# Kernel tuning notes

Measured on AMD Instinct MI355X. Metric: run time of the kernel, lower is better.

The kernel has to match this reference:

```python
import jax, jax.numpy as jnp
import numpy as np

LN_EPS = 1e-5

def _mha(xq, xkv, in_w, in_b, out_w, out_b, n_heads):
    # torch nn.MultiheadAttention, batch_first=True, dropout=0
    B, S, d = xq.shape
    T = xkv.shape[1]
    dh = d // n_heads
    wq, wk, wv = jnp.split(in_w, 3, axis=0)   # each [d, d]
    bq, bk, bv = jnp.split(in_b, 3)
    q = (xq @ wq.T + bq).reshape(B, S, n_heads, dh).transpose(0, 2, 1, 3)
    k = (xkv @ wk.T + bk).reshape(B, T, n_heads, dh).transpose(0, 2, 1, 3)
    v = (xkv @ wv.T + bv).reshape(B, T, n_heads, dh).transpose(0, 2, 1, 3)
    scores = jnp.einsum('bhsd,bhtd->bhst', q, k) / jnp.sqrt(jnp.asarray(dh, xq.dtype))
    attn = jax.nn.softmax(scores, axis=-1)    # explicit [B,H,S,T] weights (need_weights=True path)
    o = jnp.einsum('bhst,bhtd->bhsd', attn, v)
    o = o.transpose(0, 2, 1, 3).reshape(B, S, d)
    return o @ out_w.T + out_b

def _ln(x, g, b):
    mu = jnp.mean(x, axis=-1, keepdims=True)
    var = jnp.mean(jnp.square(x - mu), axis=-1, keepdims=True)
    return (x - mu) / jnp.sqrt(var + LN_EPS) * g + b

def setup_inputs() -> dict:
    key = jax.random.key(0)
    B, S, T, d, ff = 4, 1024, 1024, 1024, 4096
    ks = jax.random.split(key, 10)
    s = 0.02
    return {
        'x': jax.random.normal(ks[0], (B, S, d), jnp.float32),
        'mem': jax.random.normal(ks[1], (B, T, d), jnp.float32),
        'sa_in_w': jax.random.normal(ks[2], (3 * d, d), jnp.float32) * s,
        'sa_in_b': jnp.zeros((3 * d,), jnp.float32),
        'sa_out_w': jax.random.normal(ks[3], (d, d), jnp.float32) * s,
        'sa_out_b': jnp.zeros((d,), jnp.float32),
        'ca_in_w': jax.random.normal(ks[4], (3 * d, d), jnp.float32) * s,
        'ca_in_b': jnp.zeros((3 * d,), jnp.float32),
        'ca_out_w': jax.random.normal(ks[5], (d, d), jnp.float32) * s,
        'ca_out_b': jnp.zeros((d,), jnp.float32),
        'ff_w1': jax.random.normal(ks[6], (ff, d), jnp.float32) * s,
        'ff_b1': jnp.zeros((ff,), jnp.float32),
        'ff_w2': jax.random.normal(ks[7], (d, ff), jnp.float32) * s,
        'ff_b2': jnp.zeros((d,), jnp.float32),
        'ln1_g': jnp.ones((d,), jnp.float32), 'ln1_b': jnp.zeros((d,), jnp.float32),
        'ln2_g': jnp.ones((d,), jnp.float32), 'ln2_b': jnp.zeros((d,), jnp.float32),
        'ln3_g': jnp.ones((d,), jnp.float32), 'ln3_b': jnp.zeros((d,), jnp.float32),
        'n_heads': 16,
    }

def reference(x, mem, sa_in_w, sa_in_b, sa_out_w, sa_out_b,
              ca_in_w, ca_in_b, ca_out_w, ca_out_b,
              ff_w1, ff_b1, ff_w2, ff_b2,
              ln1_g, ln1_b, ln2_g, ln2_b, ln3_g, ln3_b, n_heads):
    sa = _mha(x, x, sa_in_w, sa_in_b, sa_out_w, sa_out_b, n_heads)
    x = _ln(x + sa, ln1_g, ln1_b)
    ca = _mha(x, mem, ca_in_w, ca_in_b, ca_out_w, ca_out_b, n_heads)
    x = _ln(x + ca, ln2_g, ln2_b)
    h = jax.nn.gelu(x @ ff_w1.T + ff_b1, approximate=False)  # torch nn.GELU default = exact erf
    ff = h @ ff_w2.T + ff_b2
    return _ln(x + ff, ln3_g, ln3_b)
```

## Files before the change

### kernel.cpp

```cpp
#include <hip/hip_runtime.h>
#include <cstddef>

#define D_MODEL 1024
#define SEQ     1024
#define BATCH   4
#define NHEAD   16
#define DH      64
#define FFDIM   4096
#define NTOK    (BATCH*SEQ)

typedef float f32x4  __attribute__((ext_vector_type(4)));
typedef short bf16x8 __attribute__((ext_vector_type(8)));

static __device__ __forceinline__ unsigned short f2bf(float x){
  union { float f; unsigned u; } v; v.f = x;
  unsigned r = v.u + 0x7fffu + ((v.u >> 16) & 1u);
  return (unsigned short)(r >> 16);
}

static __device__ __forceinline__ float bf2f(unsigned short h){
  union { unsigned u; float f; } v; v.u = ((unsigned)h) << 16; return v.f;
}

static __device__ __forceinline__ void gl_lds16(const void* g, void* l){
  __builtin_amdgcn_global_load_lds((const __attribute__((address_space(1))) void*)g,
                                   (__attribute__((address_space(3))) void*)l, 16, 0, 0);
}

static __device__ __forceinline__ int2 swz_tile(int gx, int RX, int RY){
  int id = blockIdx.y * gx + blockIdx.x;
  int x = id & 7, s = id >> 3;
  int nrx = gx / RX;
  int bx = (x % nrx) * RX + (s % RX);
  int by = (x / nrx) * RY + (s / RX);
  return make_int2(bx, by);
}

struct CvtJobs {
  const float* src[8];
  unsigned short* dst[8];
  int n[8];
};

__global__ __launch_bounds__(256) void cvt_kernel(CvtJobs jobs){
  int seg = blockIdx.y;
  const float* s = jobs.src[seg];
  unsigned short* d = jobs.dst[seg];
  int n = jobs.n[seg];
  int stride = gridDim.x * 256 * 4;
  for (int i = (blockIdx.x*256 + threadIdx.x)*4; i < n; i += stride){
    float4 v = *(const float4*)(s + i);
    ushort4 o;
    o.x = f2bf(v.x); o.y = f2bf(v.y); o.z = f2bf(v.z); o.w = f2bf(v.w);
    *(ushort4*)(d + i) = o;
  }
}

static __device__ __forceinline__ int cidx(int row, int col){
  return row*128 + (((col >> 3) ^ (row & 15)) << 3) + (col & 7);
}

template<int EPI>
static __device__ __forceinline__ void gemm_core(
    unsigned short* smem,
    const unsigned short* __restrict__ A,
    const unsigned short* __restrict__ B,
    const float* __restrict__ bias,
    void* __restrict__ out0,
    unsigned short* __restrict__ vt,
    int N, int K, int kbeg, int kend, int row0, int col0,
    int split, int ldout)
{
  unsigned short* As = smem;
  unsigned short* Bs = smem + 128*64;
  const int tid  = threadIdx.x;
  const int w    = tid >> 6, lane = tid & 63;
  const int quad = lane >> 4, l15 = lane & 15;
  const int lr   = lane >> 3, lc = lane & 7;
  const int csrc = lc ^ lr;
  const int sw   = l15 & 7;
  const int wm = (w >> 1) * 64, wn = (w & 1) * 64;

  f32x4 acc[4][4];
  const f32x4 zero4 = {0.f, 0.f, 0.f, 0.f};
  #pragma unroll
  for (int i=0;i<4;i++)
    #pragma unroll
    for (int j=0;j<4;j++)
      acc[i][j] = zero4;

  const unsigned short* Ag = A + (size_t)(row0 + lr)*K + csrc*8;
  const unsigned short* Bg = B + (size_t)(col0 + lr)*K + csrc*8;

  for (int k0 = kbeg; k0 < kend; k0 += 64){
    #pragma unroll
    for (int i=0;i<4;i++){
      gl_lds16(Ag + (size_t)(i*32 + w*8)*K + k0, &As[i*2048 + w*512]);
      gl_lds16(Bg + (size_t)(i*32 + w*8)*K + k0, &Bs[i*2048 + w*512]);
    }
    __syncthreads();
    #pragma unroll
    for (int ks=0; ks<2; ks++){
      bf16x8 af[4], bfr[4];
      #pragma unroll
      for (int i=0;i<4;i++)
        af[i] = *(const bf16x8*)&As[(wm + i*16 + l15)*64 + ((ks*4 + quad) ^ sw)*8];
      #pragma unroll
      for (int j=0;j<4;j++)
        bfr[j] = *(const bf16x8*)&Bs[(wn + j*16 + l15)*64 + ((ks*4 + quad) ^ sw)*8];
      #pragma unroll
      for (int i=0;i<4;i++)
        #pragma unroll
        for (int j=0;j<4;j++)
          acc[i][j] = __builtin_amdgcn_mfma_f32_16x16x32_bf16(af[i], bfr[j], acc[i][j], 0, 0, 0);
    }
    __syncthreads();
  }

  float bj[4];
  #pragma unroll
  for (int j=0;j<4;j++) bj[j] = bias[col0 + wn + j*16 + l15];

  const bool vtile = (EPI == 5) && (col0 >= split);
  unsigned short* Cs = smem;

  #pragma unroll
  for (int i=0;i<4;i++){
    #pragma unroll
    for (int r=0;r<4;r++){
      int lrow = wm + i*16 + quad*4 + r;
      #pragma unroll
      for (int j=0;j<4;j++){
        int lcol = wn + j*16 + l15;
        float v = acc[i][j][r] + bj[j];
        if (EPI == 2){
          float t = 0.7978845608f * (v + 0.044715f * v * v * v);
          float e = __expf(2.f * t);
          float th = 1.f - 2.f * __builtin_amdgcn_rcpf(e + 1.f);
          v = 0.5f * v * (1.f + th);
        }
        if (vtile) Cs[cidx(lcol, lrow)] = f2bf(v);
        else       Cs[cidx(lrow, lcol)] = f2bf(v);
      }
    }
  }
  __syncthreads();

  const int ld = (EPI == 5) ? ldout : N;
  #pragma unroll
  for (int p=0;p<2;p++){
    int c = p*64 + (tid >> 2);
    unsigned short* dst;
    if (!vtile){
      dst = (unsigned short*)out0 + (size_t)(row0 + c)*ld + col0;
    } else {
      int colg = (col0 - split) + c;
      int hh = colg >> 6, dd = colg & 63;
      int bb = row0 >> 10, t0 = row0 & 1023;
      dst = vt + ((size_t)(bb*NHEAD + hh)*DH + dd)*SEQ + t0;
    }
    #pragma unroll
    for (int k=0;k<4;k++){
      int m = (tid & 3) + k*4;
      bf16x8 val = *(const bf16x8*)&Cs[c*128 + ((m ^ (c & 15)) << 3)];
      *(bf16x8*)(dst + m*8) = val;
    }
  }
}

template<int EPI>
__global__ __launch_bounds__(256) void gemm_swz(
    const unsigned short* A, const unsigned short* B, const float* bias,
    void* out0, int N, int K, int RX, int RY)
{
  __shared__ __align__(16) unsigned short smem[2*128*64];
  int2 t = swz_tile(gridDim.x, RX, RY);
  gemm_core<EPI>(smem, A, B, bias, out0, nullptr, N, K, 0, K,
                 t.y*128, t.x*128, 0, 0);
}

__global__ __launch_bounds__(256) void gemm_kv(
    const unsigned short* xb, const unsigned short* memb,
    const unsigned short* wsa, const unsigned short* wca,
    const float* bsa, const float* bca,
    unsigned short* ksa, unsigned short* vtsa,
    unsigned short* kca, unsigned short* vtca)
{
  __shared__ __align__(16) unsigned short smem[2*128*64];
  const int id = blockIdx.x;
  const bool sa = id < 512;
  const int hid = id & 511;
  const int x = hid & 7, s = hid >> 3;
  const int bx = (x & 1)*8 + (s & 7);
  const int by = (x >> 1)*8 + (s >> 3);
  gemm_core<5>(smem, sa ? xb : memb, sa ? wsa : wca, sa ? bsa : bca,
               sa ? ksa : kca, sa ? vtsa : vtca,
               2048, 1024, 0, 1024, by*128, bx*128, 1024, 1024);
}

__global__ __launch_bounds__(256) void gemm_split(
    const unsigned short* A, const unsigned short* B, const float* bias,
    unsigned short* outA, unsigned short* outB, int N, int K)
{
  __shared__ __align__(16) unsigned short smem[2*128*64];
  int2 t = swz_tile(gridDim.x, 4, 8);
  int kseg = K >> 1;
  int kbeg = blockIdx.z * kseg;
  unsigned short* o = blockIdx.z ? outB : outA;
  gemm_core<1>(smem, A, B, bias, o, nullptr, N, K, kbeg, kbeg + kseg,
               t.y*128, t.x*128, 0, 0);
}

__global__ __launch_bounds__(256) void gemm_split4(
    const unsigned short* A, const unsigned short* B, const float* bias,
    unsigned short* o0, unsigned short* o1, unsigned short* o2, unsigned short* o3,
    int N, int K)
{
  __shared__ __align__(16) unsigned short smem[2*128*64];
  int2 t = swz_tile(gridDim.x, 4, 8);
  int kseg = K >> 2;
  int kbeg = blockIdx.z * kseg;
  unsigned short* o = (blockIdx.z == 0) ? o0 : (blockIdx.z == 1) ? o1
                    : (blockIdx.z == 2) ? o2 : o3;
  gemm_core<1>(smem, A, B, bias, o, nullptr, N, K, kbeg, kbeg + kseg,
               t.y*128, t.x*128, 0, 0);
}

__global__ __launch_bounds__(256) void attn_kernel(
    const unsigned short* __restrict__ Xa,
    const unsigned short* __restrict__ Wq,
    const float* __restrict__ bq,
    const unsigned short* __restrict__ Kp,
    const unsigned short* __restrict__ Vt,
    unsigned short* __restrict__ O)
{
  __shared__ __align__(16) unsigned short Qs[128*64];
  __shared__ __align__(16) unsigned short Ks[64*64];
  __shared__ __align__(16) unsigned short Vs[64*64];
  __shared__ __align__(16) unsigned short Ps[4*32*72];

  const int tid  = threadIdx.x;
  const int w    = tid >> 6, lane = tid & 63;
  const int quad = lane >> 4, l15 = lane & 15;
  const int lr   = lane >> 3, lc = lane & 7;
  const int csrc = lc ^ lr;
  const int sw   = l15 & 7;
  const int id = blockIdx.x;
  const int xc = id & 7, s = id >> 3;
  const int bh = xc*8 + (s >> 3), qt = s & 7;
  const int b = bh >> 4, h = bh & 15;
  const int q0   = qt * 128;
  const int tok0 = b * SEQ;
  const int hoff = h * DH;

  f32x4 qacc[2][4];
  const f32x4 zero4 = {0.f, 0.f, 0.f, 0.f};
  #pragma unroll
  for (int qi=0;qi<2;qi++)
    #pragma unroll
    for (int dj=0;dj<4;dj++)
      qacc[qi][dj] = zero4;

  const unsigned short* Ag = Xa + (size_t)(tok0 + q0 + lr)*1024 + csrc*8;
  const unsigned short* Wg = Wq + (size_t)(hoff + lr)*1024 + csrc*8;

  for (int k0 = 0; k0 < 1024; k0 += 64){
    #pragma unroll
    for (int i=0;i<4;i++)
      gl_lds16(Ag + (size_t)(i*32 + w*8)*1024 + k0, &Qs[i*2048 + w*512]);
    #pragma unroll
    for (int i=0;i<2;i++)
      gl_lds16(Wg + (size_t)(i*32 + w*8)*1024 + k0, &Ks[i*2048 + w*512]);
    __syncthreads();
    #pragma unroll
    for (int ks=0; ks<2; ks++){
      bf16x8 af[2], bfr[4];
      #pragma unroll
      for (int qi=0;qi<2;qi++)
        af[qi] = *(const bf16x8*)&Qs[(w*32 + qi*16 + l15)*64 + ((ks*4 + quad) ^ sw)*8];
      #pragma unroll
      for (int dj=0;dj<4;dj++)
        bfr[dj] = *(const bf16x8*)&Ks[(dj*16 + l15)*64 + ((ks*4 + quad) ^ sw)*8];
      #pragma unroll
      for (int qi=0;qi<2;qi++)
        #pragma unroll
        for (int dj=0;dj<4;dj++)
          qacc[qi][dj] = __builtin_amdgcn_mfma_f32_16x16x32_bf16(af[qi], bfr[dj], qacc[qi][dj], 0, 0, 0);
    }
    __syncthreads();
  }

  {
    float biasv[4];
    #pragma unroll
    for (int dj=0;dj<4;dj++) biasv[dj] = bq[hoff + dj*16 + l15];
    #pragma unroll
    for (int qi=0;qi<2;qi++)
      #pragma unroll
      for (int dj=0;dj<4;dj++)
        #pragma unroll
        for (int r=0;r<4;r++){
          int q = w*32 + qi*16 + quad*4 + r;
          int d = dj*16 + l15;
          Qs[q*64 + (((d>>3) ^ (q&7))<<3) + (d&7)] = f2bf(qacc[qi][dj][r] + biasv[dj]);
        }
  }
  __syncthreads();

  bf16x8 qb[2][2];
  #pragma unroll
  for (int qi=0;qi<2;qi++){
    int row = w*32 + qi*16 + l15;
    qb[qi][0] = *(const bf16x8*)&Qs[row*64 + ((0 + quad) ^ sw)*8];
    qb[qi][1] = *(const bf16x8*)&Qs[row*64 + ((4 + quad) ^ sw)*8];
  }

  float lsum[2] = {0.f, 0.f};
  f32x4 oacc[2][4];
  #pragma unroll
  for (int qi=0;qi<2;qi++)
    #pragma unroll
    for (int dt=0;dt<4;dt++)
      oacc[qi][dt] = zero4;

  unsigned short* pw = &Ps[w*32*72];

  for (int kc = 0; kc < SEQ/64; ++kc){
    __syncthreads();
    #pragma unroll
    for (int i=0;i<2;i++){
      int r = i*32 + w*8 + lr;
      gl_lds16(Kp + (size_t)(tok0 + kc*64 + r)*1024 + hoff + csrc*8, &Ks[i*2048 + w*512]);
      gl_lds16(Vt + ((size_t)bh*DH + r)*SEQ + kc*64 + csrc*8,        &Vs[i*2048 + w*512]);
    }
    __syncthreads();

    #pragma unroll
    for (int tj=0;tj<4;tj++){
      bf16x8 ka0 = *(const bf16x8*)&Ks[(tj*16 + l15)*64 + ((0 + quad) ^ sw)*8];
      bf16x8 ka1 = *(const bf16x8*)&Ks[(tj*16 + l15)*64 + ((4 + quad) ^ sw)*8];
      #pragma unroll
      for (int qi=0;qi<2;qi++){
        f32x4 z = zero4;
        __builtin_amdgcn_s_setprio(1);
        z = __builtin_amdgcn_mfma_f32_16x16x32_bf16(ka0, qb[qi][0], z, 0, 0, 0);
        z = __builtin_amdgcn_mfma_f32_16x16x32_bf16(ka1, qb[qi][1], z, 0, 0, 0);
        __builtin_amdgcn_s_setprio(0);
        float p0 = __expf(z[0] * 0.125f);
        float p1 = __expf(z[1] * 0.125f);
        float p2 = __expf(z[2] * 0.125f);
        float p3 = __expf(z[3] * 0.125f);
        lsum[qi] += (p0 + p1) + (p2 + p3);
        short4 pk;
        pk.x = (short)f2bf(p0); pk.y = (short)f2bf(p1);
        pk.z = (short)f2bf(p2); pk.w = (short)f2bf(p3);
        *(short4*)&pw[(qi*16 + l15)*72 + tj*16 + quad*4] = pk;
      }
    }

    __builtin_amdgcn_s_setprio(1);
    #pragma unroll
    for (int qi=0;qi<2;qi++){
      bf16x8 pa0 = *(const bf16x8*)&pw[(qi*16 + l15)*72 + quad*8];
      bf16x8 pa1 = *(const bf16x8*)&pw[(qi*16 + l15)*72 + 32 + quad*8];
      #pragma unroll
      for (int dt=0;dt<4;dt++){
        bf16x8 vb0 = *(const bf16x8*)&Vs[(dt*16 + l15)*64 + ((0 + quad) ^ sw)*8];
        bf16x8 vb1 = *(const bf16x8*)&Vs[(dt*16 + l15)*64 + ((4 + quad) ^ sw)*8];
        oacc[qi][dt] = __builtin_amdgcn_mfma_f32_16x16x32_bf16(pa0, vb0, oacc[qi][dt], 0, 0, 0);
        oacc[qi][dt] = __builtin_amdgcn_mfma_f32_16x16x32_bf16(pa1, vb1, oacc[qi][dt], 0, 0, 0);
      }
    }
    __builtin_amdgcn_s_setprio(0);
  }

  #pragma unroll
  for (int qi=0;qi<2;qi++){
    lsum[qi] += __shfl_xor(lsum[qi], 16);
    lsum[qi] += __shfl_xor(lsum[qi], 32);
  }

  __syncthreads();
  unsigned short* OB = Ps;
  #pragma unroll
  for (int qi=0;qi<2;qi++){
    #pragma unroll
    for (int r=0;r<4;r++){
      float lv = __shfl(lsum[qi], quad*4 + r);
      float rinv = __builtin_amdgcn_rcpf(lv);
      int q = w*32 + qi*16 + quad*4 + r;
      #pragma unroll
      for (int dt=0;dt<4;dt++){
        int d = dt*16 + l15;
        OB[q*64 + (((d>>3) ^ (q&7))<<3) + (d&7)] = f2bf(oacc[qi][dt][r] * rinv);
      }
    }
  }
  __syncthreads();
  {
    int q = tid >> 1;
    unsigned short* dst = O + (size_t)(tok0 + q0 + q)*D_MODEL + hoff;
    #pragma unroll
    for (int k=0;k<4;k++){
      int m = (tid & 1)*4 + k;
      bf16x8 val = *(const bf16x8*)&OB[q*64 + ((m ^ (q & 7)) << 3)];
      *(bf16x8*)(dst + m*8) = val;
    }
  }
}

__global__ __launch_bounds__(256) void ln_kernel(
    const float* __restrict__ resid,
    const unsigned short* __restrict__ d1,
    const unsigned short* __restrict__ d2,
    const unsigned short* __restrict__ d3,
    const unsigned short* __restrict__ d4,
    const float* __restrict__ g, const float* __restrict__ beta,
    float* __restrict__ outf, unsigned short* __restrict__ outb)
{
  const int row = blockIdx.x;
  const int t = threadIdx.x;
  const size_t base = (size_t)row * D_MODEL;
  float4 a = *(const float4*)(resid + base + t*4);
  ushort4 p4 = *(const ushort4*)(d1 + base + t*4);
  ushort4 q4 = *(const ushort4*)(d2 + base + t*4);
  float v0 = a.x + bf2f(p4.x) + bf2f(q4.x);
  float v1 = a.y + bf2f(p4.y) + bf2f(q4.y);
  float v2 = a.z + bf2f(p4.z) + bf2f(q4.z);
  float v3 = a.w + bf2f(p4.w) + bf2f(q4.w);
  if (d3){
    ushort4 r4 = *(const ushort4*)(d3 + base + t*4);
    ushort4 s4 = *(const ushort4*)(d4 + base + t*4);
    v0 += bf2f(r4.x) + bf2f(s4.x);
    v1 += bf2f(r4.y) + bf2f(s4.y);
    v2 += bf2f(r4.z) + bf2f(s4.z);
    v3 += bf2f(r4.w) + bf2f(s4.w);
  }
  float s1 = v0+v1+v2+v3;
  float s2 = v0*v0+v1*v1+v2*v2+v3*v3;
  #pragma unroll
  for (int off=32; off>0; off>>=1){
    s1 += __shfl_down(s1, off);
    s2 += __shfl_down(s2, off);
  }
  __shared__ float red[8];
  const int wid = t >> 6;
  if ((t & 63) == 0){ red[wid*2] = s1; red[wid*2+1] = s2; }
  __syncthreads();
  s1 = red[0]+red[2]+red[4]+red[6];
  s2 = red[1]+red[3]+red[5]+red[7];
  float mean = s1 * (1.f/1024.f);
  float var  = s2 * (1.f/1024.f) - mean*mean;
  float rstd = rsqrtf(var + 1e-5f);
  float4 gg = *(const float4*)(g + t*4);
  float4 bb = *(const float4*)(beta + t*4);
  float y0 = (v0-mean)*rstd*gg.x + bb.x;
  float y1 = (v1-mean)*rstd*gg.y + bb.y;
  float y2 = (v2-mean)*rstd*gg.z + bb.z;
  float y3 = (v3-mean)*rstd*gg.w + bb.w;
  if (outf) *(float4*)(outf + base + t*4) = make_float4(y0,y1,y2,y3);
  if (outb){
    ushort4 o;
    o.x = f2bf(y0); o.y = f2bf(y1); o.z = f2bf(y2); o.w = f2bf(y3);
    *(ushort4*)(outb + base + t*4) = o;
  }
}

extern "C" void kernel_launch(void* const* d_in, const int* in_sizes, int n_in,
                              void* d_out, int out_size, void* d_ws, size_t ws_size,
                              hipStream_t stream)
{
  const float* x        = (const float*)d_in[0];
  const float* mem      = (const float*)d_in[1];
  const float* sa_in_w  = (const float*)d_in[2];
  const float* sa_in_b  = (const float*)d_in[3];
  const float* sa_out_w = (const float*)d_in[4];
  const float* sa_out_b = (const float*)d_in[5];
  const float* ca_in_w  = (const float*)d_in[6];
  const float* ca_in_b  = (const float*)d_in[7];
  const float* ca_out_w = (const float*)d_in[8];
  const float* ca_out_b = (const float*)d_in[9];
  const float* ff_w1    = (const float*)d_in[10];
  const float* ff_b1    = (const float*)d_in[11];
  const float* ff_w2    = (const float*)d_in[12];
  const float* ff_b2    = (const float*)d_in[13];
  const float* ln1_g    = (const float*)d_in[14];
  const float* ln1_b    = (const float*)d_in[15];
  const float* ln2_g    = (const float*)d_in[16];
  const float* ln2_b    = (const float*)d_in[17];
  const float* ln3_g    = (const float*)d_in[18];
  const float* ln3_b    = (const float*)d_in[19];

  char* base = (char*)d_ws;
  size_t off = 0;
  auto alloc = [&](size_t bytes) -> void* {
    void* r = base + off;
    off += (bytes + 255) & ~(size_t)255;
    return r;
  };
  unsigned short* xb     = (unsigned short*)alloc((size_t)NTOK*1024*2);
  unsigned short* memb   = (unsigned short*)alloc((size_t)NTOK*1024*2);
  unsigned short* wsain  = (unsigned short*)alloc((size_t)3072*1024*2);
  unsigned short* wsaout = (unsigned short*)alloc((size_t)1024*1024*2);
  unsigned short* wcain  = (unsigned short*)alloc((size_t)3072*1024*2);
  unsigned short* wcaout = (unsigned short*)alloc((size_t)1024*1024*2);
  unsigned short* wff1   = (unsigned short*)alloc((size_t)4096*1024*2);
  unsigned short* wff2   = (unsigned short*)alloc((size_t)4096*1024*2);
  unsigned short* qkvbuf = (unsigned short*)alloc((size_t)NTOK*3072*2);
  unsigned short* attnb  = (unsigned short*)alloc((size_t)NTOK*1024*2);
  float*          proj   = (float*)alloc((size_t)NTOK*1024*4);
  float*          x1f    = (float*)alloc((size_t)NTOK*1024*4);
  unsigned short* x1b    = (unsigned short*)alloc((size_t)NTOK*1024*2);
  float*          x2f    = (float*)alloc((size_t)NTOK*1024*4);
  unsigned short* x2b    = (unsigned short*)alloc((size_t)NTOK*1024*2);

  unsigned short* ksa  = qkvbuf;
  unsigned short* vtsa = qkvbuf + (size_t)NTOK*1024;
  unsigned short* kca  = qkvbuf + (size_t)NTOK*2048;
  unsigned short* vtca = (unsigned short*)x2f;
  unsigned short* hbuf = qkvbuf;
  unsigned short* pA   = (unsigned short*)proj;
  unsigned short* pB   = (unsigned short*)xb;
  unsigned short* q0p  = (unsigned short*)proj;
  unsigned short* q1p  = (unsigned short*)proj + (size_t)NTOK*1024;
  unsigned short* q2p  = (unsigned short*)x1f;
  unsigned short* q3p  = (unsigned short*)x1f + (size_t)NTOK*1024;

  CvtJobs jobs;
  jobs.src[0]=x;        jobs.dst[0]=xb;     jobs.n[0]=NTOK*1024;
  jobs.src[1]=mem;      jobs.dst[1]=memb;   jobs.n[1]=NTOK*1024;
  jobs.src[2]=sa_in_w;  jobs.dst[2]=wsain;  jobs.n[2]=3072*1024;
  jobs.src[3]=sa_out_w; jobs.dst[3]=wsaout; jobs.n[3]=1024*1024;
  jobs.src[4]=ca_in_w;  jobs.dst[4]=wcain;  jobs.n[4]=3072*1024;
  jobs.src[5]=ca_out_w; jobs.dst[5]=wcaout; jobs.n[5]=1024*1024;
  jobs.src[6]=ff_w1;    jobs.dst[6]=wff1;   jobs.n[6]=4096*1024;
  jobs.src[7]=ff_w2;    jobs.dst[7]=wff2;   jobs.n[7]=4096*1024;
  cvt_kernel<<<dim3(1024,8), 256, 0, stream>>>(jobs);

  gemm_kv<<<1024, 256, 0, stream>>>(xb, memb,
                                    wsain + (size_t)1024*1024, wcain + (size_t)1024*1024,
                                    sa_in_b + 1024, ca_in_b + 1024,
                                    ksa, vtsa, kca, vtca);

  attn_kernel<<<512, 256, 0, stream>>>(xb, wsain, sa_in_b, ksa, vtsa, attnb);
  gemm_split<<<dim3(8,32,2), 256, 0, stream>>>(attnb, wsaout, sa_out_b, pA, pB, 1024, 1024);
  ln_kernel<<<NTOK, 256, 0, stream>>>(x, pA, pB, nullptr, nullptr, ln1_g, ln1_b, x1f, x1b);

  attn_kernel<<<512, 256, 0, stream>>>(x1b, wcain, ca_in_b, kca, vtca, attnb);
  gemm_split<<<dim3(8,32,2), 256, 0, stream>>>(attnb, wcaout, ca_out_b, pA, pB, 1024, 1024);
  ln_kernel<<<NTOK, 256, 0, stream>>>(x1f, pA, pB, nullptr, nullptr, ln2_g, ln2_b, x2f, x2b);

  gemm_swz<2><<<dim3(32,32), 256, 0, stream>>>(x2b, wff1, ff_b1, hbuf, 4096, 1024, 8, 16);
  gemm_split4<<<dim3(8,32,4), 256, 0, stream>>>(hbuf, wff2, ff_b2, q0p, q1p, q2p, q3p, 1024, 4096);
  ln_kernel<<<NTOK, 256, 0, stream>>>(x2f, q0p, q1p, q2p, q3p, ln3_g, ln3_b, (float*)d_out, nullptr);
}
```

Measured before the change: 461.6 us.

## Double-buffer Q-projection and K/V tile loads in fused attention kernel

```diff
diff --git a/kernel.cpp b/kernel.cpp
--- a/kernel.cpp
+++ b/kernel.cpp
@@ -26,6 +26,10 @@
   __builtin_amdgcn_global_load_lds((const __attribute__((address_space(1))) void*)g,
                                    (__attribute__((address_space(3))) void*)l, 16, 0, 0);
 }
+
+#define WAITV(n) asm volatile("s_waitcnt vmcnt(" #n ")" ::: "memory")
+#define SBAR()   __builtin_amdgcn_s_barrier()
+#define SCHED0() __builtin_amdgcn_sched_barrier(0)
 
 static __device__ __forceinline__ int2 swz_tile(int gx, int RX, int RY){
   int id = blockIdx.y * gx + blockIdx.x;
@@ -253,8 +257,9 @@
   const int tok0 = b * SEQ;
   const int hoff = h * DH;
 
+  const f32x4 zero4 = {0.f, 0.f, 0.f, 0.f};
+
   f32x4 qacc[2][4];
-  const f32x4 zero4 = {0.f, 0.f, 0.f, 0.f};
   #pragma unroll
   for (int qi=0;qi<2;qi++)
     #pragma unroll
@@ -264,30 +269,45 @@
   const unsigned short* Ag = Xa + (size_t)(tok0 + q0 + lr)*1024 + csrc*8;
   const unsigned short* Wg = Wq + (size_t)(hoff + lr)*1024 + csrc*8;
 
-  for (int k0 = 0; k0 < 1024; k0 += 64){
+  auto stageQ = [&](int k0, unsigned short* dA, unsigned short* dW){
     #pragma unroll
     for (int i=0;i<4;i++)
-      gl_lds16(Ag + (size_t)(i*32 + w*8)*1024 + k0, &Qs[i*2048 + w*512]);
+      gl_lds16(Ag + (size_t)(i*32 + w*8)*1024 + k0, &dA[i*2048 + w*512]);
     #pragma unroll
     for (int i=0;i<2;i++)
-      gl_lds16(Wg + (size_t)(i*32 + w*8)*1024 + k0, &Ks[i*2048 + w*512]);
-    __syncthreads();
+      gl_lds16(Wg + (size_t)(i*32 + w*8)*1024 + k0, &dW[i*2048 + w*512]);
+  };
+
+  auto computeQ = [&](const unsigned short* As_, const unsigned short* Ws_){
     #pragma unroll
     for (int ks=0; ks<2; ks++){
       bf16x8 af[2], bfr[4];
       #pragma unroll
       for (int qi=0;qi<2;qi++)
-        af[qi] = *(const bf16x8*)&Qs[(w*32 + qi*16 + l15)*64 + ((ks*4 + quad) ^ sw)*8];
+        af[qi] = *(const bf16x8*)&As_[(w*32 + qi*16 + l15)*64 + ((ks*4 + quad) ^ sw)*8];
       #pragma unroll
       for (int dj=0;dj<4;dj++)
-        bfr[dj] = *(const bf16x8*)&Ks[(dj*16 + l15)*64 + ((ks*4 + quad) ^ sw)*8];
+        bfr[dj] = *(const bf16x8*)&Ws_[(dj*16 + l15)*64 + ((ks*4 + quad) ^ sw)*8];
       #pragma unroll
       for (int qi=0;qi<2;qi++)
         #pragma unroll
         for (int dj=0;dj<4;dj++)
           qacc[qi][dj] = __builtin_amdgcn_mfma_f32_16x16x32_bf16(af[qi], bfr[dj], qacc[qi][dj], 0, 0, 0);
     }
-    __syncthreads();
+  };
+
+  stageQ(0, Qs, Ks);
+  for (int t=0; t<8; t++){
+    const int k0 = t*128;
+    stageQ(k0+64, Ps, Vs);
+    WAITV(6); SBAR(); SCHED0();
+    computeQ(Qs, Ks);
+    SCHED0(); SBAR();
+    if (t < 7){ stageQ(k0+128, Qs, Ks); WAITV(6); }
+    else      { WAITV(0); }
+    SBAR(); SCHED0();
+    computeQ(Ps, Vs);
+    SCHED0(); SBAR();
   }
 
   {
@@ -314,6 +334,7 @@
     qb[qi][0] = *(const bf16x8*)&Qs[row*64 + ((0 + quad) ^ sw)*8];
     qb[qi][1] = *(const bf16x8*)&Qs[row*64 + ((4 + quad) ^ sw)*8];
   }
+  __syncthreads();
 
   float lsum[2] = {0.f, 0.f};
   f32x4 oacc[2][4];
@@ -324,21 +345,23 @@
       oacc[qi][dt] = zero4;
 
   unsigned short* pw = &Ps[w*32*72];
-
-  for (int kc = 0; kc < SEQ/64; ++kc){
-    __syncthreads();
+  unsigned short* K1 = Qs;
+  unsigned short* V1 = Qs + 64*64;
+
+  auto stageKV = [&](int kc, unsigned short* kb, unsigned short* vb){
     #pragma unroll
     for (int i=0;i<2;i++){
       int r = i*32 + w*8 + lr;
-      gl_lds16(Kp + (size_t)(tok0 + kc*64 + r)*1024 + hoff + csrc*8, &Ks[i*2048 + w*512]);
-      gl_lds16(Vt + ((size_t)bh*DH + r)*SEQ + kc*64 + csrc*8,        &Vs[i*2048 + w*512]);
-    }
-    __syncthreads();
-
+      gl_lds16(Kp + (size_t)(tok0 + kc*64 + r)*1024 + hoff + csrc*8, &kb[i*2048 + w*512]);
+      gl_lds16(Vt + ((size_t)bh*DH + r)*SEQ + kc*64 + csrc*8,        &vb[i*2048 + w*512]);
+    }
+  };
+
+  auto computeKC = [&](const unsigned short* kb, const unsigned short* vb){
     #pragma unroll
     for (int tj=0;tj<4;tj++){
-      bf16x8 ka0 = *(const bf16x8*)&Ks[(tj*16 + l15)*64 + ((0 + quad) ^ sw)*8];
-      bf16x8 ka1 = *(const bf16x8*)&Ks[(tj*16 + l15)*64 + ((4 + quad) ^ sw)*8];
+      bf16x8 ka0 = *(const bf16x8*)&kb[(tj*16 + l15)*64 + ((0 + quad) ^ sw)*8];
+      bf16x8 ka1 = *(const bf16x8*)&kb[(tj*16 + l15)*64 + ((4 + quad) ^ sw)*8];
       #pragma unroll
       for (int qi=0;qi<2;qi++){
         f32x4 z = zero4;
@@ -357,7 +380,6 @@
         *(short4*)&pw[(qi*16 + l15)*72 + tj*16 + quad*4] = pk;
       }
     }
-
     __builtin_amdgcn_s_setprio(1);
     #pragma unroll
     for (int qi=0;qi<2;qi++){
@@ -365,13 +387,27 @@
       bf16x8 pa1 = *(const bf16x8*)&pw[(qi*16 + l15)*72 + 32 + quad*8];
       #pragma unroll
       for (int dt=0;dt<4;dt++){
-        bf16x8 vb0 = *(const bf16x8*)&Vs[(dt*16 + l15)*64 + ((0 + quad) ^ sw)*8];
-        bf16x8 vb1 = *(const bf16x8*)&Vs[(dt*16 + l15)*64 + ((4 + quad) ^ sw)*8];
+        bf16x8 vb0 = *(const bf16x8*)&vb[(dt*16 + l15)*64 + ((0 + quad) ^ sw)*8];
+        bf16x8 vb1 = *(const bf16x8*)&vb[(dt*16 + l15)*64 + ((4 + quad) ^ sw)*8];
         oacc[qi][dt] = __builtin_amdgcn_mfma_f32_16x16x32_bf16(pa0, vb0, oacc[qi][dt], 0, 0, 0);
         oacc[qi][dt] = __builtin_amdgcn_mfma_f32_16x16x32_bf16(pa1, vb1, oacc[qi][dt], 0, 0, 0);
       }
     }
     __builtin_amdgcn_s_setprio(0);
+  };
+
+  stageKV(0, Ks, Vs);
+  for (int t=0; t<8; t++){
+    const int kcA = 2*t;
+    stageKV(kcA+1, K1, V1);
+    WAITV(4); SBAR(); SCHED0();
+    computeKC(Ks, Vs);
+    SCHED0(); SBAR();
+    if (t < 7){ stageKV(kcA+2, Ks, Vs); WAITV(4); }
+    else      { WAITV(0); }
+    SBAR(); SCHED0();
+    computeKC(K1, V1);
+    SCHED0(); SBAR();
   }
 
   #pragma unroll
```

Result: no change. 466.6 us (+1.1%).

## Use 256x256 tile GEMM with 512 threads for KV, FFN1 and FFN2

Applied to the files above, without the earlier changes.

```diff
diff --git a/kernel.cpp b/kernel.cpp
--- a/kernel.cpp
+++ b/kernel.cpp
@@ -26,6 +26,11 @@
   __builtin_amdgcn_global_load_lds((const __attribute__((address_space(1))) void*)g,
                                    (__attribute__((address_space(3))) void*)l, 16, 0, 0);
 }
+
+#define WAITV(n) asm volatile("s_waitcnt vmcnt(" #n ")" ::: "memory")
+#define WAITL0() asm volatile("s_waitcnt lgkmcnt(0)" ::: "memory")
+#define SBAR()   __builtin_amdgcn_s_barrier()
+#define SCHED0() __builtin_amdgcn_sched_barrier(0)
 
 static __device__ __forceinline__ int2 swz_tile(int gx, int RX, int RY){
   int id = blockIdx.y * gx + blockIdx.x;
@@ -121,17 +126,152 @@
   #pragma unroll
   for (int j=0;j<4;j++) bj[j] = bias[col0 + wn + j*16 + l15];
 
+  unsigned short* Cs = smem;
+
+  #pragma unroll
+  for (int i=0;i<4;i++){
+    #pragma unroll
+    for (int r=0;r<4;r++){
+      int lrow = wm + i*16 + quad*4 + r;
+      #pragma unroll
+      for (int j=0;j<4;j++){
+        int lcol = wn + j*16 + l15;
+        float v = acc[i][j][r] + bj[j];
+        Cs[cidx(lrow, lcol)] = f2bf(v);
+      }
+    }
+  }
+  __syncthreads();
+
+  const int ld = N;
+  #pragma unroll
+  for (int p=0;p<2;p++){
+    int c = p*64 + (tid >> 2);
+    unsigned short* dst = (unsigned short*)out0 + (size_t)(row0 + c)*ld + col0;
+    #pragma unroll
+    for (int k=0;k<4;k++){
+      int m = (tid & 3) + k*4;
+      bf16x8 val = *(const bf16x8*)&Cs[c*128 + ((m ^ (c & 15)) << 3)];
+      *(bf16x8*)(dst + m*8) = val;
+    }
+  }
+}
+
+__global__ __launch_bounds__(256) void gemm_split(
+    const unsigned short* A, const unsigned short* B, const float* bias,
+    unsigned short* outA, unsigned short* outB, int N, int K)
+{
+  __shared__ __align__(16) unsigned short smem[2*128*64];
+  int2 t = swz_tile(gridDim.x, 4, 8);
+  int kseg = K >> 1;
+  int kbeg = blockIdx.z * kseg;
+  unsigned short* o = blockIdx.z ? outB : outA;
+  gemm_core<1>(smem, A, B, bias, o, nullptr, N, K, kbeg, kbeg + kseg,
+               t.y*128, t.x*128, 0, 0);
+}
+
+template<int EPI>
+static __device__ __forceinline__ void gemm256_core(
+    unsigned short* smem,
+    const unsigned short* __restrict__ A,
+    const unsigned short* __restrict__ B,
+    const float* __restrict__ bias,
+    void* __restrict__ out0,
+    unsigned short* __restrict__ vt,
+    int N, int K, int kbeg, int kend, int row0, int col0,
+    int split, int ldout)
+{
+  const int tid  = threadIdx.x;
+  const int w    = tid >> 6, lane = tid & 63;
+  const int quad = lane >> 4, l15 = lane & 15;
+  const int lr   = lane >> 3, lc = lane & 7;
+  const int csrc = lc ^ lr;
+  const int sw   = l15 & 7;
+  const int wr   = w >> 2, wc = w & 3;
+
+  f32x4 acc[8][4];
+  const f32x4 zero4 = {0.f, 0.f, 0.f, 0.f};
+  #pragma unroll
+  for (int i=0;i<8;i++)
+    #pragma unroll
+    for (int j=0;j<4;j++)
+      acc[i][j] = zero4;
+
+  const unsigned short* Ag = A + (size_t)(row0 + lr)*K + csrc*8;
+  const unsigned short* Bg = B + (size_t)(col0 + lr)*K + csrc*8;
+
+  auto stageT = [&](int k0, unsigned short* dst){
+    #pragma unroll
+    for (int i=0;i<4;i++)
+      gl_lds16(Ag + (size_t)(i*64 + w*8)*K + k0, dst + i*4096 + w*512);
+    #pragma unroll
+    for (int i=0;i<4;i++)
+      gl_lds16(Bg + (size_t)(i*64 + w*8)*K + k0, dst + 256*64 + i*4096 + w*512);
+  };
+
+  auto computeT = [&](const unsigned short* buf){
+    const unsigned short* As_ = buf;
+    const unsigned short* Bs_ = buf + 256*64;
+    #pragma unroll
+    for (int ks=0; ks<2; ks++){
+      const int ch = ((ks*4 + quad) ^ sw)*8;
+      bf16x8 bfr[4], af[4];
+      #pragma unroll
+      for (int j=0;j<4;j++)
+        bfr[j] = *(const bf16x8*)&Bs_[(wc*64 + j*16 + l15)*64 + ch];
+      #pragma unroll
+      for (int i=0;i<4;i++)
+        af[i] = *(const bf16x8*)&As_[(wr*128 + i*16 + l15)*64 + ch];
+      __builtin_amdgcn_s_setprio(1);
+      #pragma unroll
+      for (int i=0;i<4;i++)
+        #pragma unroll
+        for (int j=0;j<4;j++)
+          acc[i][j] = __builtin_amdgcn_mfma_f32_16x16x32_bf16(af[i], bfr[j], acc[i][j], 0, 0, 0);
+      __builtin_amdgcn_s_setprio(0);
+      #pragma unroll
+      for (int i=0;i<4;i++)
+        af[i] = *(const bf16x8*)&As_[(wr*128 + (i+4)*16 + l15)*64 + ch];
+      __builtin_amdgcn_s_setprio(1);
+      #pragma unroll
+      for (int i=0;i<4;i++)
+        #pragma unroll
+        for (int j=0;j<4;j++)
+          acc[i+4][j] = __builtin_amdgcn_mfma_f32_16x16x32_bf16(af[i], bfr[j], acc[i+4][j], 0, 0, 0);
+      __builtin_amdgcn_s_setprio(0);
+    }
+  };
+
+  const int NT = (kend - kbeg) >> 6;
+  stageT(kbeg,      smem);
+  stageT(kbeg + 64, smem + 32768);
+  WAITV(8); SBAR(); SCHED0();
+
+  for (int t=0; t<NT; t++){
+    unsigned short* cur = smem + (t&1)*32768;
+    computeT(cur);
+    WAITL0(); SCHED0();
+    SBAR();
+    if (t+2 < NT){ stageT(kbeg + (t+2)*64, cur); WAITV(8); }
+    else if (t+1 < NT){ WAITV(0); }
+    SBAR(); SCHED0();
+  }
+
+  float bj[4];
+  #pragma unroll
+  for (int j=0;j<4;j++) bj[j] = bias[col0 + wc*64 + j*16 + l15];
+
   const bool vtile = (EPI == 5) && (col0 >= split);
   unsigned short* Cs = smem;
 
   #pragma unroll
-  for (int i=0;i<4;i++){
+  for (int i=0;i<8;i++){
     #pragma unroll
     for (int r=0;r<4;r++){
-      int lrow = wm + i*16 + quad*4 + r;
+      int lrow = wr*128 + i*16 + quad*4 + r;
       #pragma unroll
       for (int j=0;j<4;j++){
-        int lcol = wn + j*16 + l15;
+        int lcol = wc*64 + j*16 + l15;
         float v = acc[i][j][r] + bj[j];
         if (EPI == 2){
           float t = 0.7978845608f * (v + 0.044715f * v * v * v);
@@ -139,17 +279,16 @@
           float th = 1.f - 2.f * __builtin_amdgcn_rcpf(e + 1.f);
           v = 0.5f * v * (1.f + th);
         }
-        if (vtile) Cs[cidx(lcol, lrow)] = f2bf(v);
-        else       Cs[cidx(lrow, lcol)] = f2bf(v);
+        int rr = vtile ? lcol : lrow, cc = vtile ? lrow : lcol;
+        Cs[rr*256 + (((cc >> 3) ^ (rr & 31)) << 3) + (cc & 7)] = f2bf(v);
       }
     }
   }
   __syncthreads();
 
   const int ld = (EPI == 5) ? ldout : N;
-  #pragma unroll
-  for (int p=0;p<2;p++){
-    int c = p*64 + (tid >> 2);
+  {
+    int c = tid >> 1;
     unsigned short* dst;
     if (!vtile){
       dst = (unsigned short*)out0 + (size_t)(row0 + c)*ld + col0;
@@ -160,70 +299,58 @@
       dst = vt + ((size_t)(bb*NHEAD + hh)*DH + dd)*SEQ + t0;
     }
     #pragma unroll
-    for (int k=0;k<4;k++){
-      int m = (tid & 3) + k*4;
-      bf16x8 val = *(const bf16x8*)&Cs[c*128 + ((m ^ (c & 15)) << 3)];
+    for (int k=0;k<16;k++){
+      int m = (tid & 1)*16 + k;
+      bf16x8 val = *(const bf16x8*)&Cs[c*256 + ((m ^ (c & 31)) << 3)];
       *(bf16x8*)(dst + m*8) = val;
     }
   }
 }
 
-template<int EPI>
-__global__ __launch_bounds__(256) void gemm_swz(
+__global__ __launch_bounds__(512, 2) void gemm256_ffn1(
     const unsigned short* A, const unsigned short* B, const float* bias,
-    void* out0, int N, int K, int RX, int RY)
-{
-  __shared__ __align__(16) unsigned short smem[2*128*64];
-  int2 t = swz_tile(gridDim.x, RX, RY);
-  gemm_core<EPI>(smem, A, B, bias, out0, nullptr, N, K, 0, K,
-                 t.y*128, t.x*128, 0, 0);
-}
-
-__global__ __launch_bounds__(256) void gemm_kv(
+    unsigned short* out0, int N, int K)
+{
+  __shared__ __align__(16) unsigned short smem[2*2*256*64];
+  int2 t = swz_tile(gridDim.x, 4, 8);
+  gemm256_core<2>(smem, A, B, bias, out0, nullptr, N, K, 0, K,
+                  t.y*256, t.x*256, 0, 0);
+}
+
+__global__ __launch_bounds__(512, 2) void gemm_kv256(
     const unsigned short* xb, const unsigned short* memb,
     const unsigned short* wsa, const unsigned short* wca,
     const float* bsa, const float* bca,
     unsigned short* ksa, unsigned short* vtsa,
     unsigned short* kca, unsigned short* vtca)
 {
-  __shared__ __align__(16) unsigned short smem[2*128*64];
+  __shared__ __align__(16) unsigned short smem[2*2*256*64];
   const int id = blockIdx.x;
-  const bool sa = id < 512;
-  const int hid = id & 511;
-  const int x = hid & 7, s = hid >> 3;
-  const int bx = (x & 1)*8 + (s & 7);
-  const int by = (x >> 1)*8 + (s >> 3);
-  gemm_core<5>(smem, sa ? xb : memb, sa ? wsa : wca, sa ? bsa : bca,
-               sa ? ksa : kca, sa ? vtsa : vtca,
-               2048, 1024, 0, 1024, by*128, bx*128, 1024, 1024);
-}
-
-__global__ __launch_bounds__(256) void gemm_split(
-    const unsigned short* A, const unsigned short* B, const float* bias,
-    unsigned short* outA, unsigned short* outB, int N, int K)
-{
-  __shared__ __align__(16) unsigned short smem[2*128*64];
-  int2 t = swz_tile(gridDim.x, 4, 8);
-  int kseg = K >> 1;
-  int kbeg = blockIdx.z * kseg;
-  unsigned short* o = blockIdx.z ? outB : outA;
-  gemm_core<1>(smem, A, B, bias, o, nullptr, N, K, kbeg, kbeg + kseg,
-               t.y*128, t.x*128, 0, 0);
-}
-
-__global__ __launch_bounds__(256) void gemm_split4(
+  const int xcd = id & 7, s = id >> 3;
+  const bool sa = s < 16;
+  const int u = sa ? s : s - 16;
+  const int bx = (xcd & 3)*2 + (u & 1);
+  const int by = (xcd >> 2)*8 + (u >> 1);
+  gemm256_core<5>(smem, sa ? xb : memb, sa ? wsa : wca, sa ? bsa : bca,
+                  sa ? ksa : kca, sa ? vtsa : vtca,
+                  2048, 1024, 0, 1024, by*256, bx*256, 1024, 1024);
+}
+
+__global__ __launch_bounds__(512, 2) void gemm256_split4(
     const unsigned short* A, const unsigned short* B, const float* bias,
     unsigned short* o0, unsigned short* o1, unsigned short* o2, unsigned short* o3,
     int N, int K)
 {
-  __shared__ __align__(16) unsigned short smem[2*128*64];
-  int2 t = swz_tile(gridDim.x, 4, 8);
-  int kseg = K >> 2;
-  int kbeg = blockIdx.z * kseg;
-  unsigned short* o = (blockIdx.z == 0) ? o0 : (blockIdx.z == 1) ? o1
-                    : (blockIdx.z == 2) ? o2 : o3;
-  gemm_core<1>(smem, A, B, bias, o, nullptr, N, K, kbeg, kbeg + kseg,
-               t.y*128, t.x*128, 0, 0);
+  __shared__ __align__(16) unsigned short smem[2*2*256*64];
+  const int id = blockIdx.x;
+  const int xcd = id & 7, s = id >> 3;
+  const int z  = xcd >> 1;
+  const int bx = s & 3;
+  const int by = (xcd & 1)*8 + (s >> 2);
+  const int kseg = K >> 2, kbeg = z * kseg;
+  unsigned short* o = (z == 0) ? o0 : (z == 1) ? o1 : (z == 2) ? o2 : o3;
+  gemm256_core<1>(smem, A, B, bias, o, nullptr, N, K, kbeg, kbeg + kseg,
+                  by*256, bx*256, 0, 0);
 }
 
 __global__ __launch_bounds__(256) void attn_kernel(
@@ -537,10 +664,10 @@
   jobs.src[7]=ff_w2;    jobs.dst[7]=wff2;   jobs.n[7]=4096*1024;
   cvt_kernel<<<dim3(1024,8), 256, 0, stream>>>(jobs);
 
-  gemm_kv<<<1024, 256, 0, stream>>>(xb, memb,
-                                    wsain + (size_t)1024*1024, wcain + (size_t)1024*1024,
-                                    sa_in_b + 1024, ca_in_b + 1024,
-                                    ksa, vtsa, kca, vtca);
+  gemm_kv256<<<256, 512, 0, stream>>>(xb, memb,
+                                      wsain + (size_t)1024*1024, wcain + (size_t)1024*1024,
+                                      sa_in_b + 1024, ca_in_b + 1024,
+                                      ksa, vtsa, kca, vtca);
 
   attn_kernel<<<512, 256, 0, stream>>>(xb, wsain, sa_in_b, ksa, vtsa, attnb);
   gemm_split<<<dim3(8,32,2), 256, 0, stream>>>(attnb, wsaout, sa_out_b, pA, pB, 1024, 1024);
@@ -550,7 +677,7 @@
   gemm_split<<<dim3(8,32,2), 256, 0, stream>>>(attnb, wcaout, ca_out_b, pA, pB, 1024, 1024);
   ln_kernel<<<NTOK, 256, 0, stream>>>(x1f, pA, pB, nullptr, nullptr, ln2_g, ln2_b, x2f, x2b);
 
-  gemm_swz<2><<<dim3(32,32), 256, 0, stream>>>(x2b, wff1, ff_b1, hbuf, 4096, 1024, 8, 16);
-  gemm_split4<<<dim3(8,32,4), 256, 0, stream>>>(hbuf, wff2, ff_b2, q0p, q1p, q2p, q3p, 1024, 4096);
+  gemm256_ffn1<<<dim3(16,16), 512, 0, stream>>>(x2b, wff1, ff_b1, hbuf, 4096, 1024);
+  gemm256_split4<<<256, 512, 0, stream>>>(hbuf, wff2, ff_b2, q0p, q1p, q2p, q3p, 1024, 4096);
   ln_kernel<<<NTOK, 256, 0, stream>>>(x2f, q0p, q1p, q2p, q3p, ln3_g, ln3_b, (float*)d_out, nullptr);
 }
```

New measurement: 482.7 us. 4.6% more time.
